# Optimization experiments

Hardware: AMD Instinct MI355X
Metric: run time of the kernel (lower is better)

Reference implementation:

```python
import jax, jax.numpy as jnp
import numpy as np

B, V, T, D, H = 8, 64, 256, 256, 8
DH = D // H
LN_EPS = 1e-5


def setup_inputs() -> dict:
    key = jax.random.key(0)
    k0, k1, k2, k3 = jax.random.split(key, 4)
    x = jax.random.normal(k0, (B, V, T + 1, D), dtype=jnp.float32)
    obs_mask = jax.random.randint(k1, (B, V, T), 0, 2).astype(bool)
    ln_w = jnp.ones((D,), jnp.float32)
    ln_b = jnp.zeros((D,), jnp.float32)
    w_qkv = jax.random.normal(k2, (3 * D, D), dtype=jnp.float32) * 0.02   # torch Linear weight (out,in), no bias
    w_proj = jax.random.normal(k3, (D, D), dtype=jnp.float32) * 0.02
    b_proj = jnp.zeros((D,), jnp.float32)
    return dict(x=x, obs_mask=obs_mask, ln_w=ln_w, ln_b=ln_b,
                w_qkv=w_qkv, w_proj=w_proj, b_proj=b_proj)


def reference(x, obs_mask, ln_w, ln_b, w_qkv, w_proj, b_proj):
    b, v, t1, d = x.shape
    h, dh = H, D // H

    # LayerNorm over last dim
    mu = jnp.mean(x, axis=-1, keepdims=True)
    var = jnp.mean(jnp.square(x - mu), axis=-1, keepdims=True)
    xn = (x - mu) * jax.lax.rsqrt(var + LN_EPS) * ln_w + ln_b

    # QKV projection: (B,V,T1,3D) -> (B,V,T1,3,H,dh)
    qkv = jnp.einsum('bvtd,ed->bvte', xn, w_qkv).reshape(b, v, t1, 3, h, dh)
    qf = qkv[:, :, :, 0]  # (B,V,T1,H,dh)
    kf = qkv[:, :, :, 1]
    vf = qkv[:, :, :, 2]

    # Queries from position 0 only: (B,H,V,dh)
    q = jnp.transpose(qf[:, :, 0], (0, 2, 1, 3))

    # Keys: masked mean over time (query token at pos 0 always observed)
    mask = jnp.concatenate([jnp.ones((b, v, 1), bool), obs_mask], axis=2)  # (B,V,T1)
    mf = mask[..., None, None].astype(kf.dtype)                            # (B,V,T1,1,1)
    cnt = jnp.clip(mask.sum(axis=2).astype(kf.dtype), 1.0)[:, :, None, None]
    k = (kf * mf).sum(axis=2) / cnt                                        # (B,V,H,dh)
    k = jnp.transpose(k, (0, 2, 1, 3))                                     # (B,H,V,dh)

    # Small cross-variable attention matrix (B,H,V,V)
    scale = dh ** -0.5
    attn = jax.nn.softmax(jnp.einsum('bhqd,bhkd->bhqk', q, k) * scale, axis=-1)

    # Values packed with temporal structure: (B,H,V,dh,T1)
    vp = jnp.transpose(vf, (0, 3, 1, 4, 2))
    out = jnp.einsum('bhqk,bhkdt->bhqdt', attn, vp)                        # (B,H,V,dh,T1)

    # Unpack back to (B,V,T1,D)
    out = jnp.transpose(out, (0, 2, 4, 1, 3)).reshape(b, v, t1, d)
    out = out @ w_proj.T + b_proj
    return x + out
```

## Files before the change

### kernel.cpp

```cpp
#include <hip/hip_runtime.h>
#include <hip/hip_bf16.h>

typedef unsigned short u16;
typedef __attribute__((ext_vector_type(8))) short short8;
typedef __attribute__((ext_vector_type(4))) float f32x4;

#define B_ 8
#define V_ 64
#define T_ 256
#define T1_ 257
#define D_ 256
#define H_ 8
#define DH_ 32

__device__ __forceinline__ u16 f2bf(float f){
  union { float f; unsigned int u; } v; v.f = f;
  unsigned int u = v.u;
  return (u16)((u + 0x7fffu + ((u >> 16) & 1u)) >> 16);
}

__global__ void k1_ln(const float* __restrict__ x, const int* __restrict__ mask,
                      const float* __restrict__ lnw, const float* __restrict__ lnb,
                      const float* __restrict__ wqkv, const float* __restrict__ wproj,
                      float* __restrict__ musig, float* __restrict__ xsum,
                      u16* __restrict__ wv, u16* __restrict__ wp){
  if (blockIdx.x >= 512){
    int j = (blockIdx.x - 512) * 512 + threadIdx.x;
    wv[j] = f2bf(wqkv[131072 + j]);
    wp[j] = f2bf(wproj[j]);
    return;
  }
  int bv = blockIdx.x;
  int tid = threadIdx.x;
  int lane = tid & 63, wid = tid >> 6;
  int half = lane >> 5, l32 = lane & 31;
  int c8 = l32 * 8;
  __shared__ float xsred[8][512];
  float4 w0 = *(const float4*)&lnw[c8], w1 = *(const float4*)&lnw[c8 + 4];
  float4 b0 = *(const float4*)&lnb[c8], b1 = *(const float4*)&lnb[c8 + 4];
  float xs[8];
  #pragma unroll
  for (int j = 0; j < 8; ++j) xs[j] = 0.f;
  for (int p = wid; p < 129; p += 8){
    int t = p * 2 + half;
    bool valid = (t < T1_);
    float4 a0 = {0.f,0.f,0.f,0.f}, a1 = {0.f,0.f,0.f,0.f};
    if (valid){
      const float* gp = &x[((long)bv * T1_ + t) * D_ + c8];
      a0 = *(const float4*)gp; a1 = *(const float4*)(gp + 4);
    }
    float s  = a0.x + a0.y + a0.z + a0.w + a1.x + a1.y + a1.z + a1.w;
    float s2 = a0.x*a0.x + a0.y*a0.y + a0.z*a0.z + a0.w*a0.w
             + a1.x*a1.x + a1.y*a1.y + a1.z*a1.z + a1.w*a1.w;
    #pragma unroll
    for (int off = 1; off < 32; off <<= 1){
      s  += __shfl_xor(s,  off, 64);
      s2 += __shfl_xor(s2, off, 64);
    }
    float mu   = s * (1.f / 256.f);
    float var  = s2 * (1.f / 256.f) - mu * mu;
    float rstd = rsqrtf(var + 1e-5f);
    if (valid){
      if (l32 == 0){
        musig[((long)bv * T1_ + t) * 2]     = mu;
        musig[((long)bv * T1_ + t) * 2 + 1] = rstd;
      }
      int m = (t == 0) ? 1 : mask[bv * T_ + (t - 1)];
      if (m){
        xs[0] += (a0.x - mu) * rstd * w0.x + b0.x;
        xs[1] += (a0.y - mu) * rstd * w0.y + b0.y;
        xs[2] += (a0.z - mu) * rstd * w0.z + b0.z;
        xs[3] += (a0.w - mu) * rstd * w0.w + b0.w;
        xs[4] += (a1.x - mu) * rstd * w1.x + b1.x;
        xs[5] += (a1.y - mu) * rstd * w1.y + b1.y;
        xs[6] += (a1.z - mu) * rstd * w1.z + b1.z;
        xs[7] += (a1.w - mu) * rstd * w1.w + b1.w;
      }
    }
  }
  #pragma unroll
  for (int j = 0; j < 8; ++j) xsred[wid][half * 256 + c8 + j] = xs[j];
  __syncthreads();
  if (tid < 256){
    float r = 0.f;
    #pragma unroll
    for (int w2 = 0; w2 < 8; ++w2) r += xsred[w2][tid] + xsred[w2][256 + tid];
    xsum[bv * D_ + tid] = r;
  }
}

__global__ void k2a_qk(const float* __restrict__ x, const int* __restrict__ mask,
                       const float* __restrict__ lnw, const float* __restrict__ lnb,
                       const float* __restrict__ wqkv,
                       const float* __restrict__ musig, const float* __restrict__ xsum,
                       float* __restrict__ qout, float* __restrict__ kout){
  int bv = blockIdx.x, tid = threadIdx.x;
  int lane = tid & 63, wid = tid >> 6;
  __shared__ __align__(16) float xn0[D_];
  __shared__ __align__(16) float xs[D_];
  __shared__ float redc[4];
  int s = mask[bv * T_ + tid];
  #pragma unroll
  for (int off = 32; off >= 1; off >>= 1) s += __shfl_down(s, off, 64);
  if (lane == 0) redc[wid] = (float)s;
  __syncthreads();
  float cnt = 1.f + redc[0] + redc[1] + redc[2] + redc[3];
  float mu = musig[((long)bv * T1_) * 2], rstd = musig[((long)bv * T1_) * 2 + 1];
  xn0[tid] = (x[((long)bv * T1_) * D_ + tid] - mu) * rstd * lnw[tid] + lnb[tid];
  xs[tid]  = xsum[bv * D_ + tid] * (1.f / cnt);
  __syncthreads();
  float4 xq = *(const float4*)&xn0[lane * 4];
  float4 xk = *(const float4*)&xs[lane * 4];
  int e0 = (blockIdx.y * 4 + wid) * 16;
  for (int i = 0; i < 16; ++i){
    int e = e0 + i;
    float4 wq4 = *(const float4*)&wqkv[(long)e * D_ + lane * 4];
    float4 wk4 = *(const float4*)&wqkv[(long)(256 + e) * D_ + lane * 4];
    float sq = xq.x*wq4.x + xq.y*wq4.y + xq.z*wq4.z + xq.w*wq4.w;
    float sk = xk.x*wk4.x + xk.y*wk4.y + xk.z*wk4.z + xk.w*wk4.w;
    #pragma unroll
    for (int off = 32; off >= 1; off >>= 1){
      sq += __shfl_down(sq, off, 64);
      sk += __shfl_down(sk, off, 64);
    }
    if (lane == 0){ qout[bv * D_ + e] = sq; kout[bv * D_ + e] = sk; }
  }
}

__global__ void k2b_attn(const float* __restrict__ q, const float* __restrict__ k,
                         u16* __restrict__ attn){
  int bh = blockIdx.x; int b = bh >> 3, h = bh & 7;
  int tid = threadIdx.x;
  int lane = tid & 63, wid = tid >> 6;
  __shared__ float qs[64][33], ks[64][33];
  #pragma unroll
  for (int j = 0; j < 2; ++j){
    int i4 = tid * 2 + j;
    int r = i4 >> 3, c4 = (i4 & 7) * 4;
    float4 vq = *(const float4*)&q[((long)(b * V_ + r)) * D_ + h * DH_ + c4];
    float4 vk = *(const float4*)&k[((long)(b * V_ + r)) * D_ + h * DH_ + c4];
    qs[r][c4] = vq.x; qs[r][c4+1] = vq.y; qs[r][c4+2] = vq.z; qs[r][c4+3] = vq.w;
    ks[r][c4] = vk.x; ks[r][c4+1] = vk.y; ks[r][c4+2] = vk.z; ks[r][c4+3] = vk.w;
  }
  __syncthreads();
  const float scale = 0.17677669529663687f;
  for (int i = blockIdx.y * 4; i < blockIdx.y * 4 + 4; ++i){
    int qr = i * 4 + wid;
    float a = 0.f;
    #pragma unroll
    for (int d = 0; d < DH_; ++d) a += qs[qr][d] * ks[lane][d];
    a *= scale;
    float mx = a;
    #pragma unroll
    for (int off = 1; off < 64; off <<= 1) mx = fmaxf(mx, __shfl_xor(mx, off, 64));
    float e = __expf(a - mx);
    float sum = e;
    #pragma unroll
    for (int off = 1; off < 64; off <<= 1) sum += __shfl_xor(sum, off, 64);
    attn[((long)bh * 64 + qr) * 64 + lane] = f2bf(e * (1.f / sum));
  }
}

__global__ __launch_bounds__(512, 6) void k3_main(
    const float* __restrict__ x, const float* __restrict__ lnw, const float* __restrict__ lnb,
    const float* __restrict__ bproj, const float* __restrict__ musig,
    const u16* __restrict__ wv, const u16* __restrict__ wp,
    const u16* __restrict__ attn, float* __restrict__ out){
  constexpr int XS = 264;
  __shared__ __align__(16) u16 Xs[64 * XS];
  __shared__ float lnw_s[D_], lnb_s[D_], bp_s[D_];
  __shared__ float ms_s[V_ * 2];

  int bt = blockIdx.x; int b = bt / T1_, t = bt % T1_;
  int tid = threadIdx.x;
  int w = tid >> 6, lane = tid & 63, lm = lane & 15, lq = lane >> 4;
  int cw = w * 32;
  int h = w;

  if (tid < 256){ lnw_s[tid] = lnw[tid]; lnb_s[tid] = lnb[tid]; bp_s[tid] = bproj[tid]; }
  else if (tid < 384){
    int i = tid - 256;
    ms_s[i] = musig[(((long)b * V_ + (i >> 1)) * T1_ + t) * 2 + (i & 1)];
  }
  __syncthreads();

  #pragma unroll
  for (int i = 0; i < 4; ++i){
    int seg = i * 512 + tid;
    int vr = seg >> 5;
    int c8 = (seg & 31) * 8;
    const float* gp = x + (((long)b * V_ + vr) * T1_ + t) * D_ + c8;
    float4 a0 = *(const float4*)gp;
    float4 a1 = *(const float4*)(gp + 4);
    float mu = ms_s[vr * 2], rs = ms_s[vr * 2 + 1];
    float av[8] = {a0.x, a0.y, a0.z, a0.w, a1.x, a1.y, a1.z, a1.w};
    union { u16 us[8]; uint4 q4; } pk;
    #pragma unroll
    for (int j = 0; j < 8; ++j)
      pk.us[j] = f2bf((av[j] - mu) * rs * lnw_s[c8 + j] + lnb_s[c8 + j]);
    *(uint4*)&Xs[vr * XS + c8] = pk.q4;
  }
  __syncthreads();

  f32x4 acc1[4][2];
  #pragma unroll
  for (int mt = 0; mt < 4; ++mt)
    #pragma unroll
    for (int nt = 0; nt < 2; ++nt) acc1[mt][nt] = (f32x4){0.f, 0.f, 0.f, 0.f};
  for (int kk = 0; kk < 8; ++kk){
    short8 af[4], bfr[2];
    #pragma unroll
    for (int mt = 0; mt < 4; ++mt)
      af[mt] = *(const short8*)&Xs[(mt * 16 + lm) * XS + kk * 32 + lq * 8];
    #pragma unroll
    for (int nt = 0; nt < 2; ++nt)
      bfr[nt] = *(const short8*)&wv[(long)(cw + nt * 16 + lm) * D_ + kk * 32 + lq * 8];
    #pragma unroll
    for (int mt = 0; mt < 4; ++mt)
      #pragma unroll
      for (int nt = 0; nt < 2; ++nt)
        acc1[mt][nt] = __builtin_amdgcn_mfma_f32_16x16x32_bf16(af[mt], bfr[nt], acc1[mt][nt], 0, 0, 0);
  }
  __syncthreads();

  u16* vtw = &Xs[w * 2048];
  #pragma unroll
  for (int mt = 0; mt < 4; ++mt)
    #pragma unroll
    for (int nt = 0; nt < 2; ++nt){
      int c  = nt * 16 + lm;
      int v8 = mt * 2 + (lq >> 1);
      int off = c * 64 + ((v8 ^ (lm & 7)) * 8) + (lq & 1) * 4;
      union { u16 us[4]; uint2 q2; } pv;
      #pragma unroll
      for (int r = 0; r < 4; ++r) pv.us[r] = f2bf(acc1[mt][nt][r]);
      *(uint2*)&vtw[off] = pv.q2;
    }

  f32x4 acc2[4][2];
  #pragma unroll
  for (int mt = 0; mt < 4; ++mt)
    #pragma unroll
    for (int nt = 0; nt < 2; ++nt) acc2[mt][nt] = (f32x4){0.f, 0.f, 0.f, 0.f};
  #pragma unroll
  for (int kk = 0; kk < 2; ++kk){
    short8 atf[4], bfr[2];
    #pragma unroll
    for (int mt = 0; mt < 4; ++mt)
      atf[mt] = *(const short8*)&attn[((long)(b * H_ + h) * 64 + mt * 16 + lm) * 64 + kk * 32 + lq * 8];
    #pragma unroll
    for (int nt = 0; nt < 2; ++nt){
      int c = nt * 16 + lm;
      int v8 = kk * 4 + lq;
      bfr[nt] = *(const short8*)&vtw[c * 64 + ((v8 ^ (lm & 7)) * 8)];
    }
    #pragma unroll
    for (int mt = 0; mt < 4; ++mt)
      #pragma unroll
      for (int nt = 0; nt < 2; ++nt)
        acc2[mt][nt] = __builtin_amdgcn_mfma_f32_16x16x32_bf16(atf[mt], bfr[nt], acc2[mt][nt], 0, 0, 0);
  }
  __syncthreads();

  #pragma unroll
  for (int mt = 0; mt < 4; ++mt)
    #pragma unroll
    for (int nt = 0; nt < 2; ++nt){
      int col = h * 32 + nt * 16 + lm;
      #pragma unroll
      for (int r = 0; r < 4; ++r){
        int row = mt * 16 + lq * 4 + r;
        Xs[row * XS + col] = f2bf(acc2[mt][nt][r]);
      }
    }
  __syncthreads();

  f32x4 acc3[4][2];
  #pragma unroll
  for (int mt = 0; mt < 4; ++mt)
    #pragma unroll
    for (int nt = 0; nt < 2; ++nt) acc3[mt][nt] = (f32x4){0.f, 0.f, 0.f, 0.f};
  for (int kk = 0; kk < 8; ++kk){
    short8 af[4], bfr[2];
    #pragma unroll
    for (int mt = 0; mt < 4; ++mt)
      af[mt] = *(const short8*)&Xs[(mt * 16 + lm) * XS + kk * 32 + lq * 8];
    #pragma unroll
    for (int nt = 0; nt < 2; ++nt)
      bfr[nt] = *(const short8*)&wp[(long)(cw + nt * 16 + lm) * D_ + kk * 32 + lq * 8];
    #pragma unroll
    for (int mt = 0; mt < 4; ++mt)
      #pragma unroll
      for (int nt = 0; nt < 2; ++nt)
        acc3[mt][nt] = __builtin_amdgcn_mfma_f32_16x16x32_bf16(af[mt], bfr[nt], acc3[mt][nt], 0, 0, 0);
  }
  #pragma unroll
  for (int mt = 0; mt < 4; ++mt)
    #pragma unroll
    for (int nt = 0; nt < 2; ++nt){
      int e = cw + nt * 16 + lm;
      #pragma unroll
      for (int r = 0; r < 4; ++r){
        int vr = mt * 16 + lq * 4 + r;
        long g = (((long)b * V_ + vr) * T1_ + t) * D_ + e;
        out[g] = acc3[mt][nt][r] + bp_s[e] + x[g];
      }
    }
}

extern "C" void kernel_launch(void* const* d_in, const int* in_sizes, int n_in,
                              void* d_out, int out_size, void* d_ws, size_t ws_size,
                              hipStream_t stream){
  const float* x     = (const float*)d_in[0];
  const int*   mask  = (const int*)d_in[1];
  const float* lnw   = (const float*)d_in[2];
  const float* lnb   = (const float*)d_in[3];
  const float* wqkv  = (const float*)d_in[4];
  const float* wproj = (const float*)d_in[5];
  const float* bproj = (const float*)d_in[6];
  float* out = (float*)d_out;
  char* ws = (char*)d_ws;
  float* musig = (float*)(ws);
  float* xsum  = (float*)(ws + 1052672);
  float* qbuf  = (float*)(ws + 1576960);
  float* kbuf  = (float*)(ws + 2101248);
  u16*   attn  = (u16*)  (ws + 2625536);
  u16*   wv    = (u16*)  (ws + 3149824);
  u16*   wp    = (u16*)  (ws + 3280896);

  k1_ln<<<640, 512, 0, stream>>>(x, mask, lnw, lnb, wqkv, wproj, musig, xsum, wv, wp);
  k2a_qk<<<dim3(512, 4), 256, 0, stream>>>(x, mask, lnw, lnb, wqkv, musig, xsum, qbuf, kbuf);
  k2b_attn<<<dim3(64, 4), 256, 0, stream>>>(qbuf, kbuf, attn);
  k3_main<<<B_ * T1_, 512, 0, stream>>>(x, lnw, lnb, bproj, musig, wv, wp, attn, out);
}
```

Before: 403.7 us.

## Process two time steps per block in main kernel to reuse weight fragments

The main fused kernel now handles two consecutive time positions per block instead of one, halving the grid size. Each weight fragment loaded from global memory (wv, wp) and each attention fragment is reused across both time slices, and LDS doubles to hold two normalized tiles. This is meant to cut redundant weight/attention loads and per-block setup overhead. In exchange it raises register pressure (launch bounds occupancy hint lowered to 4), doubles shared memory, and pads the last block with a clamped duplicate/zero slot for the odd T1.

```diff
diff --git a/kernel.cpp b/kernel.cpp
--- a/kernel.cpp
+++ b/kernel.cpp
@@ -161,151 +161,199 @@
   }
 }
 
-__global__ __launch_bounds__(512, 6) void k3_main(
+__global__ __launch_bounds__(512, 4) void k3_main(
     const float* __restrict__ x, const float* __restrict__ lnw, const float* __restrict__ lnb,
     const float* __restrict__ bproj, const float* __restrict__ musig,
     const u16* __restrict__ wv, const u16* __restrict__ wp,
     const u16* __restrict__ attn, float* __restrict__ out){
   constexpr int XS = 264;
-  __shared__ __align__(16) u16 Xs[64 * XS];
+  constexpr int TSL = 64 * XS;
+  __shared__ __align__(16) u16 Xs[2 * TSL];
   __shared__ float lnw_s[D_], lnb_s[D_], bp_s[D_];
-  __shared__ float ms_s[V_ * 2];
-
-  int bt = blockIdx.x; int b = bt / T1_, t = bt % T1_;
+  __shared__ float ms_s[2][V_][2];
+
+  int bt = blockIdx.x; int b = bt / 129, ty = bt % 129;
+  int t0 = ty * 2;
   int tid = threadIdx.x;
   int w = tid >> 6, lane = tid & 63, lm = lane & 15, lq = lane >> 4;
   int cw = w * 32;
   int h = w;
 
   if (tid < 256){ lnw_s[tid] = lnw[tid]; lnb_s[tid] = lnb[tid]; bp_s[tid] = bproj[tid]; }
-  else if (tid < 384){
+  else {
     int i = tid - 256;
-    ms_s[i] = musig[(((long)b * V_ + (i >> 1)) * T1_ + t) * 2 + (i & 1)];
-  }
-  __syncthreads();
-
-  #pragma unroll
-  for (int i = 0; i < 4; ++i){
+    int tslot = i >> 7, vr = (i >> 1) & 63, sel = i & 1;
+    int t = t0 + tslot; if (t > 256) t = 256;
+    ms_s[tslot][vr][sel] = musig[(((long)b * V_ + vr) * T1_ + t) * 2 + sel];
+  }
+  __syncthreads();
+
+  #pragma unroll
+  for (int i = 0; i < 8; ++i){
     int seg = i * 512 + tid;
-    int vr = seg >> 5;
+    int vr2 = seg >> 5;
+    int tslot = vr2 >> 6, vr = vr2 & 63;
     int c8 = (seg & 31) * 8;
-    const float* gp = x + (((long)b * V_ + vr) * T1_ + t) * D_ + c8;
-    float4 a0 = *(const float4*)gp;
-    float4 a1 = *(const float4*)(gp + 4);
-    float mu = ms_s[vr * 2], rs = ms_s[vr * 2 + 1];
+    int t = t0 + tslot;
+    float4 a0 = {0.f,0.f,0.f,0.f}, a1 = {0.f,0.f,0.f,0.f};
+    if (t < T1_){
+      const float* gp = x + (((long)b * V_ + vr) * T1_ + t) * D_ + c8;
+      a0 = *(const float4*)gp;
+      a1 = *(const float4*)(gp + 4);
+    }
+    float mu = ms_s[tslot][vr][0], rs = ms_s[tslot][vr][1];
     float av[8] = {a0.x, a0.y, a0.z, a0.w, a1.x, a1.y, a1.z, a1.w};
     union { u16 us[8]; uint4 q4; } pk;
     #pragma unroll
     for (int j = 0; j < 8; ++j)
       pk.us[j] = f2bf((av[j] - mu) * rs * lnw_s[c8 + j] + lnb_s[c8 + j]);
-    *(uint4*)&Xs[vr * XS + c8] = pk.q4;
-  }
-  __syncthreads();
-
-  f32x4 acc1[4][2];
-  #pragma unroll
-  for (int mt = 0; mt < 4; ++mt)
-    #pragma unroll
-    for (int nt = 0; nt < 2; ++nt) acc1[mt][nt] = (f32x4){0.f, 0.f, 0.f, 0.f};
+    *(uint4*)&Xs[tslot * TSL + vr * XS + c8] = pk.q4;
+  }
+  __syncthreads();
+
+  f32x4 acc1[2][4][2];
+  #pragma unroll
+  for (int tt = 0; tt < 2; ++tt)
+    #pragma unroll
+    for (int mt = 0; mt < 4; ++mt)
+      #pragma unroll
+      for (int nt = 0; nt < 2; ++nt) acc1[tt][mt][nt] = (f32x4){0.f, 0.f, 0.f, 0.f};
   for (int kk = 0; kk < 8; ++kk){
-    short8 af[4], bfr[2];
-    #pragma unroll
-    for (int mt = 0; mt < 4; ++mt)
-      af[mt] = *(const short8*)&Xs[(mt * 16 + lm) * XS + kk * 32 + lq * 8];
+    short8 bfr[2];
     #pragma unroll
     for (int nt = 0; nt < 2; ++nt)
       bfr[nt] = *(const short8*)&wv[(long)(cw + nt * 16 + lm) * D_ + kk * 32 + lq * 8];
     #pragma unroll
+    for (int tt = 0; tt < 2; ++tt){
+      short8 af[4];
+      #pragma unroll
+      for (int mt = 0; mt < 4; ++mt)
+        af[mt] = *(const short8*)&Xs[tt * TSL + (mt * 16 + lm) * XS + kk * 32 + lq * 8];
+      #pragma unroll
+      for (int mt = 0; mt < 4; ++mt)
+        #pragma unroll
+        for (int nt = 0; nt < 2; ++nt)
+          acc1[tt][mt][nt] = __builtin_amdgcn_mfma_f32_16x16x32_bf16(af[mt], bfr[nt], acc1[tt][mt][nt], 0, 0, 0);
+    }
+  }
+  unsigned int pw[2][4][2][2];
+  #pragma unroll
+  for (int tt = 0; tt < 2; ++tt)
+    #pragma unroll
     for (int mt = 0; mt < 4; ++mt)
       #pragma unroll
       for (int nt = 0; nt < 2; ++nt)
-        acc1[mt][nt] = __builtin_amdgcn_mfma_f32_16x16x32_bf16(af[mt], bfr[nt], acc1[mt][nt], 0, 0, 0);
-  }
-  __syncthreads();
-
-  u16* vtw = &Xs[w * 2048];
-  #pragma unroll
-  for (int mt = 0; mt < 4; ++mt)
-    #pragma unroll
-    for (int nt = 0; nt < 2; ++nt){
-      int c  = nt * 16 + lm;
-      int v8 = mt * 2 + (lq >> 1);
-      int off = c * 64 + ((v8 ^ (lm & 7)) * 8) + (lq & 1) * 4;
-      union { u16 us[4]; uint2 q2; } pv;
-      #pragma unroll
-      for (int r = 0; r < 4; ++r) pv.us[r] = f2bf(acc1[mt][nt][r]);
-      *(uint2*)&vtw[off] = pv.q2;
-    }
-
-  f32x4 acc2[4][2];
-  #pragma unroll
-  for (int mt = 0; mt < 4; ++mt)
-    #pragma unroll
-    for (int nt = 0; nt < 2; ++nt) acc2[mt][nt] = (f32x4){0.f, 0.f, 0.f, 0.f};
-  #pragma unroll
-  for (int kk = 0; kk < 2; ++kk){
-    short8 atf[4], bfr[2];
-    #pragma unroll
-    for (int mt = 0; mt < 4; ++mt)
-      atf[mt] = *(const short8*)&attn[((long)(b * H_ + h) * 64 + mt * 16 + lm) * 64 + kk * 32 + lq * 8];
-    #pragma unroll
-    for (int nt = 0; nt < 2; ++nt){
-      int c = nt * 16 + lm;
-      int v8 = kk * 4 + lq;
-      bfr[nt] = *(const short8*)&vtw[c * 64 + ((v8 ^ (lm & 7)) * 8)];
-    }
-    #pragma unroll
-    for (int mt = 0; mt < 4; ++mt)
-      #pragma unroll
-      for (int nt = 0; nt < 2; ++nt)
-        acc2[mt][nt] = __builtin_amdgcn_mfma_f32_16x16x32_bf16(atf[mt], bfr[nt], acc2[mt][nt], 0, 0, 0);
-  }
-  __syncthreads();
-
-  #pragma unroll
-  for (int mt = 0; mt < 4; ++mt)
-    #pragma unroll
-    for (int nt = 0; nt < 2; ++nt){
-      int col = h * 32 + nt * 16 + lm;
-      #pragma unroll
-      for (int r = 0; r < 4; ++r){
-        int row = mt * 16 + lq * 4 + r;
-        Xs[row * XS + col] = f2bf(acc2[mt][nt][r]);
-      }
-    }
-  __syncthreads();
-
-  f32x4 acc3[4][2];
-  #pragma unroll
-  for (int mt = 0; mt < 4; ++mt)
-    #pragma unroll
-    for (int nt = 0; nt < 2; ++nt) acc3[mt][nt] = (f32x4){0.f, 0.f, 0.f, 0.f};
+        #pragma unroll
+        for (int p = 0; p < 2; ++p)
+          pw[tt][mt][nt][p] = (unsigned int)f2bf(acc1[tt][mt][nt][2*p])
+                            | ((unsigned int)f2bf(acc1[tt][mt][nt][2*p+1]) << 16);
+  __syncthreads();
+
+  u16* vtw = &Xs[w * 4224];
+  #pragma unroll
+  for (int tt = 0; tt < 2; ++tt)
+    #pragma unroll
+    for (int mt = 0; mt < 4; ++mt)
+      #pragma unroll
+      for (int nt = 0; nt < 2; ++nt){
+        int c  = nt * 16 + lm;
+        int v8 = mt * 2 + (lq >> 1);
+        int off = tt * 2048 + c * 64 + ((v8 ^ (lm & 7)) * 8) + (lq & 1) * 4;
+        union { unsigned int wq[2]; uint2 q2; } pv;
+        pv.wq[0] = pw[tt][mt][nt][0]; pv.wq[1] = pw[tt][mt][nt][1];
+        *(uint2*)&vtw[off] = pv.q2;
+      }
+
+  short8 atf[2][4];
+  #pragma unroll
+  for (int kk = 0; kk < 2; ++kk)
+    #pragma unroll
+    for (int mt = 0; mt < 4; ++mt)
+      atf[kk][mt] = *(const short8*)&attn[((long)(b * H_ + h) * 64 + mt * 16 + lm) * 64 + kk * 32 + lq * 8];
+  f32x4 acc2[2][4][2];
+  #pragma unroll
+  for (int tt = 0; tt < 2; ++tt)
+    #pragma unroll
+    for (int mt = 0; mt < 4; ++mt)
+      #pragma unroll
+      for (int nt = 0; nt < 2; ++nt) acc2[tt][mt][nt] = (f32x4){0.f, 0.f, 0.f, 0.f};
+  #pragma unroll
+  for (int kk = 0; kk < 2; ++kk)
+    #pragma unroll
+    for (int tt = 0; tt < 2; ++tt){
+      short8 bfr[2];
+      #pragma unroll
+      for (int nt = 0; nt < 2; ++nt){
+        int c = nt * 16 + lm;
+        int v8 = kk * 4 + lq;
+        bfr[nt] = *(const short8*)&vtw[tt * 2048 + c * 64 + ((v8 ^ (lm & 7)) * 8)];
+      }
+      #pragma unroll
+      for (int mt = 0; mt < 4; ++mt)
+        #pragma unroll
+        for (int nt = 0; nt < 2; ++nt)
+          acc2[tt][mt][nt] = __builtin_amdgcn_mfma_f32_16x16x32_bf16(atf[kk][mt], bfr[nt], acc2[tt][mt][nt], 0, 0, 0);
+    }
+  __syncthreads();
+
+  #pragma unroll
+  for (int tt = 0; tt < 2; ++tt)
+    #pragma unroll
+    for (int mt = 0; mt < 4; ++mt)
+      #pragma unroll
+      for (int nt = 0; nt < 2; ++nt){
+        int col = h * 32 + nt * 16 + lm;
+        #pragma unroll
+        for (int r = 0; r < 4; ++r){
+          int row = mt * 16 + lq * 4 + r;
+          Xs[tt * TSL + row * XS + col] = f2bf(acc2[tt][mt][nt][r]);
+        }
+      }
+  __syncthreads();
+
+  f32x4 acc3[2][4][2];
+  #pragma unroll
+  for (int tt = 0; tt < 2; ++tt)
+    #pragma unroll
+    for (int mt = 0; mt < 4; ++mt)
+      #pragma unroll
+      for (int nt = 0; nt < 2; ++nt) acc3[tt][mt][nt] = (f32x4){0.f, 0.f, 0.f, 0.f};
   for (int kk = 0; kk < 8; ++kk){
-    short8 af[4], bfr[2];
-    #pragma unroll
-    for (int mt = 0; mt < 4; ++mt)
-      af[mt] = *(const short8*)&Xs[(mt * 16 + lm) * XS + kk * 32 + lq * 8];
+    short8 bfr[2];
     #pragma unroll
     for (int nt = 0; nt < 2; ++nt)
       bfr[nt] = *(const short8*)&wp[(long)(cw + nt * 16 + lm) * D_ + kk * 32 + lq * 8];
     #pragma unroll
-    for (int mt = 0; mt < 4; ++mt)
-      #pragma unroll
-      for (int nt = 0; nt < 2; ++nt)
-        acc3[mt][nt] = __builtin_amdgcn_mfma_f32_16x16x32_bf16(af[mt], bfr[nt], acc3[mt][nt], 0, 0, 0);
-  }
-  #pragma unroll
-  for (int mt = 0; mt < 4; ++mt)
-    #pragma unroll
-    for (int nt = 0; nt < 2; ++nt){
-      int e = cw + nt * 16 + lm;
-      #pragma unroll
-      for (int r = 0; r < 4; ++r){
-        int vr = mt * 16 + lq * 4 + r;
-        long g = (((long)b * V_ + vr) * T1_ + t) * D_ + e;
-        out[g] = acc3[mt][nt][r] + bp_s[e] + x[g];
-      }
-    }
+    for (int tt = 0; tt < 2; ++tt){
+      short8 af[4];
+      #pragma unroll
+      for (int mt = 0; mt < 4; ++mt)
+        af[mt] = *(const short8*)&Xs[tt * TSL + (mt * 16 + lm) * XS + kk * 32 + lq * 8];
+      #pragma unroll
+      for (int mt = 0; mt < 4; ++mt)
+        #pragma unroll
+        for (int nt = 0; nt < 2; ++nt)
+          acc3[tt][mt][nt] = __builtin_amdgcn_mfma_f32_16x16x32_bf16(af[mt], bfr[nt], acc3[tt][mt][nt], 0, 0, 0);
+    }
+  }
+  #pragma unroll
+  for (int tt = 0; tt < 2; ++tt){
+    int t = t0 + tt;
+    if (t < T1_){
+      #pragma unroll
+      for (int mt = 0; mt < 4; ++mt)
+        #pragma unroll
+        for (int nt = 0; nt < 2; ++nt){
+          int e = cw + nt * 16 + lm;
+          #pragma unroll
+          for (int r = 0; r < 4; ++r){
+            int vr = mt * 16 + lq * 4 + r;
+            long g = (((long)b * V_ + vr) * T1_ + t) * D_ + e;
+            out[g] = acc3[tt][mt][nt][r] + bp_s[e] + x[g];
+          }
+        }
+    }
+  }
 }
 
 extern "C" void kernel_launch(void* const* d_in, const int* in_sizes, int n_in,
@@ -331,5 +379,5 @@
   k1_ln<<<640, 512, 0, stream>>>(x, mask, lnw, lnb, wqkv, wproj, musig, xsum, wv, wp);
   k2a_qk<<<dim3(512, 4), 256, 0, stream>>>(x, mask, lnw, lnb, wqkv, musig, xsum, qbuf, kbuf);
   k2b_attn<<<dim3(64, 4), 256, 0, stream>>>(qbuf, kbuf, attn);
-  k3_main<<<B_ * T1_, 512, 0, stream>>>(x, lnw, lnb, bproj, musig, wv, wp, attn, out);
-}
+  k3_main<<<B_ * 129, 512, 0, stream>>>(x, lnw, lnb, bproj, musig, wv, wp, attn, out);
+}
```

Result: faster. 391.6 us (-3.0%).
